# Kernel optimization log

Hardware: AMD Instinct MI355X
Metric: run time of the kernel (lower is better)

Reference implementation:

```python
import jax, jax.numpy as jnp
import numpy as np

NUM_EMBEDDINGS = 8192
EMBEDDING_DIM = 256
COMMITMENT_WEIGHT = 0.25
EMA_DECAY = 0.99
EPSILON = 1e-05


def setup_inputs() -> dict:
    key = jax.random.key(0)
    k1, k2 = jax.random.split(key)
    z = jax.random.normal(k1, (8, 4096, EMBEDDING_DIM), dtype=jnp.float32)
    # xavier-uniform-ish codebook init
    limit = np.sqrt(6.0 / (NUM_EMBEDDINGS + EMBEDDING_DIM))
    embeddings = jax.random.uniform(
        k2, (NUM_EMBEDDINGS, EMBEDDING_DIM), dtype=jnp.float32,
        minval=-limit, maxval=limit)
    ema_cluster_size = jnp.zeros((NUM_EMBEDDINGS,), dtype=jnp.float32)
    ema_embed_sum = embeddings.copy()
    return {
        'z': z,
        'embeddings': embeddings,
        'ema_cluster_size': ema_cluster_size,
        'ema_embed_sum': ema_embed_sum,
    }


def reference(z, embeddings, ema_cluster_size, ema_embed_sum):
    input_shape = z.shape
    D = input_shape[-1]
    z_flat = z.reshape(-1, D)                                  # [N, D]

    # Squared euclidean distances via expansion: ||z||^2 + ||e||^2 - 2 z.e
    z_sq = jnp.sum(z_flat * z_flat, axis=1, keepdims=True)     # [N, 1]
    e_sq = jnp.sum(embeddings * embeddings, axis=1)            # [K]
    ze = jnp.matmul(z_flat, embeddings.T)                      # [N, K]
    distances = z_sq + e_sq - 2.0 * ze                          # [N, K]
    indices = jnp.argmin(distances, axis=1)                    # [N] int

    z_q_flat = embeddings[indices]                             # [N, D] gather
    z_q = z_q_flat.reshape(input_shape)

    # commitment loss = mse(stop_grad(z_q), z)
    diff = jax.lax.stop_gradient(z_q) - z
    commitment_loss = jnp.mean(diff * diff) * COMMITMENT_WEIGHT

    # straight-through estimator
    z_q_st = z + jax.lax.stop_gradient(z_q - z)

    # EMA codebook update (functional version of the in-place buffer update)
    ones = jnp.ones_like(indices, dtype=embeddings.dtype)
    cluster_size = jax.ops.segment_sum(ones, indices, num_segments=NUM_EMBEDDINGS)
    embed_sum = jax.ops.segment_sum(z_flat, indices, num_segments=NUM_EMBEDDINGS)
    new_ema_cluster_size = EMA_DECAY * ema_cluster_size + (1.0 - EMA_DECAY) * cluster_size
    new_ema_embed_sum = EMA_DECAY * ema_embed_sum + (1.0 - EMA_DECAY) * embed_sum
    new_embeddings = new_ema_embed_sum / (new_ema_cluster_size[:, None] + EPSILON)

    indices_out = indices.reshape(input_shape[:-1])
    return (z_q_st, indices_out, commitment_loss,
            new_embeddings, new_ema_cluster_size, new_ema_embed_sum)
```

## Files before the change

kernel.cpp:

```cpp
#include <hip/hip_runtime.h>
#include <hip/hip_bf16.h>
#include <math.h>

#define N_TOK   32768
#define DIM     256
#define KC      8192

#define OUT_ZQ    0
#define OUT_IDX   8388608
#define OUT_LOSS  8421376
#define OUT_NEMB  8421377
#define OUT_CS    10518529
#define OUT_SUM   10526721

#define MARGIN  5e-3f
#define FLAGCAP 8192

typedef __attribute__((ext_vector_type(8))) __bf16 bf16x8;
typedef __attribute__((ext_vector_type(4))) float f32x4;

__device__ __forceinline__ void gload16(const void* g, void* l) {
  __builtin_amdgcn_global_load_lds((const __attribute__((address_space(1))) void*)g,
                                   (__attribute__((address_space(3))) void*)l, 16, 0, 0);
}

__device__ __forceinline__ float np_sumsq256(const float* __restrict__ p, int lane) {
  const int l = lane & 15;
  const int h = l >> 3;
  const int j = l & 7;
  const float* a = p + h * 128 + j;
  float x = a[0];
  float r = __fmul_rn(x, x);
  #pragma unroll
  for (int i = 1; i < 16; ++i) {
    x = a[8 * i];
    r = __fadd_rn(r, __fmul_rn(x, x));
  }
  r = __fadd_rn(r, __shfl_down(r, 1));
  r = __fadd_rn(r, __shfl_down(r, 2));
  r = __fadd_rn(r, __shfl_down(r, 4));
  float hi = __shfl(r, (lane & 48) | 8);
  return __fadd_rn(r, hi);
}

__global__ void vq_prep(const float* __restrict__ emb, float* __restrict__ esq,
                        short* __restrict__ esp2) {
  const int t = threadIdx.x;
  const int code = blockIdx.x * 8 + (t >> 5);
  const int p = t & 31, j = p >> 2, g = p & 3;
  const float* src = emb + (size_t)code * DIM + j * 32 + g * 8;
  const float4 v0 = *(const float4*)src;
  const float4 v1 = *(const float4*)(src + 4);
  const float xf[8] = {v0.x, v0.y, v0.z, v0.w, v1.x, v1.y, v1.z, v1.w};
  bf16x8 hb;
  #pragma unroll
  for (int e = 0; e < 8; ++e) hb[e] = (__bf16)xf[e];
  const int c = code & 15, sub = (code >> 4) & 3, ct = code >> 6;
  const int slot = (g + (c >> 1)) & 3;
  char* dst = (char*)esp2 + (size_t)ct * 32768 + ((sub * 8 + j) << 10) + c * 64 + slot * 16;
  *(bf16x8*)dst = hb;
  if (t < 128) {
    const int code2 = blockIdx.x * 8 + (t >> 4);
    const float s = np_sumsq256(emb + (size_t)code2 * DIM, t & 63);
    if ((t & 15) == 0) esq[code2] = s;
  }
}

__global__ void vq_transpose(const float* __restrict__ emb, float* __restrict__ embT) {
  __shared__ float t[64][65];
  const int tid = threadIdx.x;
  const int bc  = blockIdx.x & 127;
  const int bk  = blockIdx.x >> 7;
  const int cc0 = bc << 6, kc0 = bk << 6;
  const int col = tid & 63, qr = tid >> 6;
  #pragma unroll
  for (int i = 0; i < 16; ++i) {
    const int row = i * 4 + qr;
    t[row][col] = emb[(size_t)(cc0 + row) * DIM + kc0 + col];
  }
  __syncthreads();
  #pragma unroll
  for (int i = 0; i < 16; ++i) {
    const int krow = i * 4 + qr;
    embT[(size_t)(kc0 + krow) * KC + cc0 + col] = t[col][krow];
  }
}

__global__ void vq_init(int* __restrict__ hist, int* __restrict__ cnt) {
  const int i = blockIdx.x * blockDim.x + threadIdx.x;
  hist[i] = 0;
  if (i == 0) cnt[0] = 0;
}

__launch_bounds__(256, 4)
__global__ void vq_mfma(const float* __restrict__ z,
                        const short* __restrict__ esp,
                        const float* __restrict__ esq,
                        float* __restrict__ pb1,
                        int* __restrict__ pi1,
                        float* __restrict__ pb2) {
  __shared__ __align__(16) char lds[32768];
  const int tid  = threadIdx.x;
  const int lane = tid & 63;
  const int w    = tid >> 6;
  const int l15  = lane & 15;
  const int g    = lane >> 4;
  const int rt   = blockIdx.x >> 1;
  const int kh   = blockIdx.x & 1;
  const int rowbase = rt * 64 + w * 16;
  const int u0 = kh * 128, u1 = u0 + 128;
  const int gx = (g + (l15 >> 1)) & 3;
  const char* espb = (const char*)esp;

#define STAGE(U, BUFB)                                                           \
  {                                                                              \
    _Pragma("unroll")                                                            \
    for (int q_ = 0; q_ < 4; ++q_) {                                             \
      const int so_ = (((w << 2) + q_) << 10);                                   \
      gload16(espb + (size_t)(U) * 16384 + so_ + (lane << 4),                    \
              (void*)(lds + (BUFB) + so_));                                      \
    }                                                                            \
  }

  STAGE(u0, 0);

  bf16x8 Ahi[8], Alo[8];
  {
    const float* zr = z + (size_t)(rowbase + l15) * DIM + g * 8;
    #pragma unroll
    for (int c = 0; c < 8; ++c) {
      const float4 v0 = *(const float4*)(zr + c * 32);
      const float4 v1 = *(const float4*)(zr + c * 32 + 4);
      const float xf[8] = {v0.x, v0.y, v0.z, v0.w, v1.x, v1.y, v1.z, v1.w};
      #pragma unroll
      for (int e = 0; e < 8; ++e) {
        __bf16 hb = (__bf16)xf[e];
        Ahi[c][e] = hb;
        Alo[c][e] = (__bf16)(xf[e] - (float)hb);
      }
    }
  }

  __syncthreads();

  float b1[4], b2[4];
  int   i1[4];
  #pragma unroll
  for (int r = 0; r < 4; ++r) { b1[r] = 3.4e38f; b2[r] = 3.4e38f; i1[r] = 0x7fffffff; }

  int bp = 0;
  for (int u = u0; u < u1; ++u) {
    if (u + 1 < u1) STAGE(u + 1, (bp ^ 1) << 14);

    const float eq0 = esq[(u << 5) + l15];
    const float eq1 = esq[(u << 5) + 16 + l15];

    f32x4 acc0 = (f32x4){0.f, 0.f, 0.f, 0.f};
    f32x4 acc1 = (f32x4){0.f, 0.f, 0.f, 0.f};

    {
      const char* base = lds + (bp << 14);
      #pragma unroll
      for (int j_ = 0; j_ < 8; ++j_) {
        const char* bq_ = base + (j_ << 10) + (l15 << 6) + (gx << 4);
        const bf16x8 bF0 = *(const bf16x8*)(bq_);
        const bf16x8 bF1 = *(const bf16x8*)(bq_ + 8192);
        acc0 = __builtin_amdgcn_mfma_f32_16x16x32_bf16(Ahi[j_], bF0, acc0, 0, 0, 0);
        acc1 = __builtin_amdgcn_mfma_f32_16x16x32_bf16(Ahi[j_], bF1, acc1, 0, 0, 0);
        acc0 = __builtin_amdgcn_mfma_f32_16x16x32_bf16(Alo[j_], bF0, acc0, 0, 0, 0);
        acc1 = __builtin_amdgcn_mfma_f32_16x16x32_bf16(Alo[j_], bF1, acc1, 0, 0, 0);
      }
    }

    const int code0 = (u << 5) + l15;
    #pragma unroll
    for (int r = 0; r < 4; ++r) {
      const float sc = fmaf(-2.f, acc0[r], eq0);
      const bool lt = sc < b1[r];
      b2[r] = fminf(b2[r], fmaxf(sc, b1[r]));
      i1[r] = lt ? code0 : i1[r];
      b1[r] = fminf(b1[r], sc);
    }
    const int code1 = code0 + 16;
    #pragma unroll
    for (int r = 0; r < 4; ++r) {
      const float sc = fmaf(-2.f, acc1[r], eq1);
      const bool lt = sc < b1[r];
      b2[r] = fminf(b2[r], fmaxf(sc, b1[r]));
      i1[r] = lt ? code1 : i1[r];
      b1[r] = fminf(b1[r], sc);
    }
    __syncthreads();
    bp ^= 1;
  }

  #pragma unroll
  for (int r = 0; r < 4; ++r) {
    float v1 = b1[r], v2 = b2[r];
    int   j1 = i1[r];
    #pragma unroll
    for (int off = 1; off < 16; off <<= 1) {
      const float o1 = __shfl_xor(v1, off);
      const int   oj = __shfl_xor(j1, off);
      const float o2 = __shfl_xor(v2, off);
      v2 = fminf(fminf(v2, o2), fmaxf(v1, o1));
      const bool tk = (o1 < v1) || (o1 == v1 && oj < j1);
      j1 = tk ? oj : j1;
      v1 = fminf(v1, o1);
    }
    if (l15 == 0) {
      const int rr = kh * N_TOK + rowbase + (g << 2) + r;
      pb1[rr] = v1; pi1[rr] = j1; pb2[rr] = v2;
    }
  }
}

__global__ void vq_merge(const float* __restrict__ pb1, const int* __restrict__ pi1,
                         const float* __restrict__ pb2, int* __restrict__ idxf,
                         int* __restrict__ flag, int* __restrict__ cnt) {
  const int gi = blockIdx.x * blockDim.x + threadIdx.x;
  const float va = pb1[gi],        vb = pb1[N_TOK + gi];
  const int   ia = pi1[gi],        ib = pi1[N_TOK + gi];
  const float v2a = pb2[gi],       v2b = pb2[N_TOK + gi];
  float v1, v2; int i1;
  if (va < vb || (va == vb && ia < ib)) { v1 = va; i1 = ia; v2 = fminf(v2a, vb); }
  else                                  { v1 = vb; i1 = ib; v2 = fminf(v2b, va); }
  idxf[gi] = i1;
  if (v2 - v1 < MARGIN) {
    const int p = atomicAdd(cnt, 1);
    if (p < FLAGCAP) flag[p] = gi;
  }
}

__global__ void vq_rescan2(const float* __restrict__ z,
                           const float* __restrict__ embT,
                           const float* __restrict__ esq,
                           const int* __restrict__ flag,
                           const int* __restrict__ cnt,
                           float* __restrict__ rpv,
                           int* __restrict__ rpi) {
  __shared__ __align__(16) float zT[DIM][16];
  __shared__ float zsq_sh[16];
  __shared__ float rv[4][16];
  __shared__ int   ri[4][16];
  __shared__ int   rown[16];
  int n = *cnt; if (n > FLAGCAP) n = FLAGCAP;
  const int tid = threadIdx.x;
  const int lane = tid & 63, wv = tid >> 6;
  const int nb = (n + 15) >> 4;
  const int ntask = nb * 8;
  for (int task = blockIdx.x; task < ntask; task += gridDim.x) {
    const int bb = task >> 3, cz = task & 7;
    __syncthreads();
    if (tid < 16) rown[tid] = flag[min(bb * 16 + tid, n - 1)];
    __syncthreads();
    #pragma unroll
    for (int rr = 0; rr < 16; ++rr) zT[tid][rr] = z[(size_t)rown[rr] * DIM + tid];
    {
      const int rr = tid >> 4;
      const float s = np_sumsq256(z + (size_t)rown[rr] * DIM, lane);
      if ((tid & 15) == 0) zsq_sh[rr] = s;
    }
    __syncthreads();

    float a[16][4];
    #pragma unroll
    for (int rr = 0; rr < 16; ++rr)
      #pragma unroll
      for (int q = 0; q < 4; ++q) a[rr][q] = 0.f;

    const int c0 = cz * 1024 + tid;
    #pragma unroll 2
    for (int k = 0; k < DIM; ++k) {
      const float* rk = embT + (size_t)k * KC + c0;
      const float e0 = rk[0], e1 = rk[256], e2 = rk[512], e3 = rk[768];
      const f32x4 z0 = *(const f32x4*)&zT[k][0];
      const f32x4 z1 = *(const f32x4*)&zT[k][4];
      const f32x4 z2 = *(const f32x4*)&zT[k][8];
      const f32x4 z3 = *(const f32x4*)&zT[k][12];
      #pragma unroll
      for (int r4 = 0; r4 < 4; ++r4) {
        a[r4][0] = fmaf(z0[r4], e0, a[r4][0]);
        a[r4][1] = fmaf(z0[r4], e1, a[r4][1]);
        a[r4][2] = fmaf(z0[r4], e2, a[r4][2]);
        a[r4][3] = fmaf(z0[r4], e3, a[r4][3]);
        a[4 + r4][0] = fmaf(z1[r4], e0, a[4 + r4][0]);
        a[4 + r4][1] = fmaf(z1[r4], e1, a[4 + r4][1]);
        a[4 + r4][2] = fmaf(z1[r4], e2, a[4 + r4][2]);
        a[4 + r4][3] = fmaf(z1[r4], e3, a[4 + r4][3]);
        a[8 + r4][0] = fmaf(z2[r4], e0, a[8 + r4][0]);
        a[8 + r4][1] = fmaf(z2[r4], e1, a[8 + r4][1]);
        a[8 + r4][2] = fmaf(z2[r4], e2, a[8 + r4][2]);
        a[8 + r4][3] = fmaf(z2[r4], e3, a[8 + r4][3]);
        a[12 + r4][0] = fmaf(z3[r4], e0, a[12 + r4][0]);
        a[12 + r4][1] = fmaf(z3[r4], e1, a[12 + r4][1]);
        a[12 + r4][2] = fmaf(z3[r4], e2, a[12 + r4][2]);
        a[12 + r4][3] = fmaf(z3[r4], e3, a[12 + r4][3]);
      }
    }

    #pragma unroll
    for (int rr = 0; rr < 16; ++rr) {
      float bv = 3.4e38f; int bi = 0x7fffffff;
      #pragma unroll
      for (int q = 0; q < 4; ++q) {
        const int code = cz * 1024 + q * 256 + tid;
        const float D = __fsub_rn(__fadd_rn(zsq_sh[rr], esq[code]), __fmul_rn(2.f, a[rr][q]));
        if (D < bv) { bv = D; bi = code; }
      }
      #pragma unroll
      for (int off = 32; off; off >>= 1) {
        const float ov = __shfl_down(bv, off);
        const int   oi = __shfl_down(bi, off);
        if (ov < bv || (ov == bv && oi < bi)) { bv = ov; bi = oi; }
      }
      if (lane == 0) { rv[wv][rr] = bv; ri[wv][rr] = bi; }
    }
    __syncthreads();
    if (tid < 16) {
      const int fi = bb * 16 + tid;
      if (fi < n) {
        float fv = rv[0][tid]; int fx = ri[0][tid];
        #pragma unroll
        for (int q = 1; q < 4; ++q)
          if (rv[q][tid] < fv || (rv[q][tid] == fv && ri[q][tid] < fx)) { fv = rv[q][tid]; fx = ri[q][tid]; }
        rpv[fi * 8 + cz] = fv; rpi[fi * 8 + cz] = fx;
      }
    }
  }
}

__global__ void vq_rmerge(const int* __restrict__ flag, const int* __restrict__ cnt,
                          const float* __restrict__ rpv, const int* __restrict__ rpi,
                          int* __restrict__ idxf) {
  int n = *cnt; if (n > FLAGCAP) n = FLAGCAP;
  const int fi = blockIdx.x * blockDim.x + threadIdx.x;
  if (fi >= n) return;
  float bv = rpv[fi * 8]; int bi = rpi[fi * 8];
  #pragma unroll
  for (int c = 1; c < 8; ++c) {
    const float v = rpv[fi * 8 + c]; const int ix = rpi[fi * 8 + c];
    if (v < bv || (v == bv && ix < bi)) { bv = v; bi = ix; }
  }
  idxf[flag[fi]] = bi;
}

__global__ void vq_gather(const float* __restrict__ z, const float* __restrict__ emb,
                          const int* __restrict__ idxf, float* __restrict__ out,
                          float* __restrict__ lossp, int* __restrict__ hist) {
  __shared__ float part[4];
  const int tid = threadIdx.x, lane = tid & 63, w = tid >> 6;
  const int row = blockIdx.x * 4 + w;
  const int code = idxf[row];
  const float4 zv = *(const float4*)(z + (size_t)row * DIM + lane * 4);
  const float4 ev = *(const float4*)(emb + (size_t)code * DIM + lane * 4);
  float4 d, o;
  d.x = ev.x - zv.x; d.y = ev.y - zv.y; d.z = ev.z - zv.z; d.w = ev.w - zv.w;
  o.x = zv.x + d.x;  o.y = zv.y + d.y;  o.z = zv.z + d.z;  o.w = zv.w + d.w;
  *(float4*)(out + OUT_ZQ + (size_t)row * DIM + lane * 4) = o;
  float sq = fmaf(d.x, d.x, fmaf(d.y, d.y, fmaf(d.z, d.z, d.w * d.w)));
  #pragma unroll
  for (int off = 32; off; off >>= 1) sq += __shfl_down(sq, off);
  if (lane == 0) {
    part[w] = sq;
    atomicAdd(hist + code, 1);
    out[OUT_IDX + row] = (float)code;
  }
  __syncthreads();
  if (tid == 0) lossp[blockIdx.x] = (part[0] + part[1]) + (part[2] + part[3]);
}

__global__ void vq_prefix(const float* __restrict__ ema_cs, int* __restrict__ hist,
                          int* __restrict__ base, int* __restrict__ cursor,
                          const float* __restrict__ lossp, float* __restrict__ out) {
  __shared__ int ps[256];
  __shared__ float lp[4];
  const int t = threadIdx.x;

  float ls = 0.f;
  #pragma unroll
  for (int j = 0; j < 8; ++j) {
    const float4 v = *(const float4*)(lossp + t * 32 + j * 4);
    ls += (v.x + v.y) + (v.z + v.w);
  }
  #pragma unroll
  for (int off = 32; off; off >>= 1) ls += __shfl_down(ls, off);
  if ((t & 63) == 0) lp[t >> 6] = ls;

  int loc[32]; int s = 0;
  #pragma unroll
  for (int j = 0; j < 32; ++j) { loc[j] = hist[t * 32 + j]; s += loc[j]; }
  ps[t] = s;
  __syncthreads();
  if (t == 0)
    out[OUT_LOSS] = 0.25f * (((lp[0] + lp[1]) + (lp[2] + lp[3])) * (1.f / 8388608.f));
  for (int off = 1; off < 256; off <<= 1) {
    const int v = (t >= off) ? ps[t - off] : 0;
    __syncthreads();
    ps[t] += v;
    __syncthreads();
  }
  int run = ps[t] - s;
  #pragma unroll
  for (int j = 0; j < 32; ++j) {
    const int i = t * 32 + j;
    base[i] = run; cursor[i] = run;
    out[OUT_CS + i] = 0.99f * ema_cs[i] + 0.01f * (float)loc[j];
    run += loc[j];
  }
}

__global__ void vq_slot(const int* __restrict__ idxf, int* __restrict__ cursor,
                        int* __restrict__ rowlist) {
  const int gi = blockIdx.x * blockDim.x + threadIdx.x;
  const int code = idxf[gi];
  const int p = atomicAdd(cursor + code, 1);
  rowlist[p] = gi;
}

__global__ void vq_embsum(const float* __restrict__ z, const float* __restrict__ ema_sum,
                          const int* __restrict__ rowlist, const int* __restrict__ base,
                          const int* __restrict__ hist, float* __restrict__ out) {
  const int code = blockIdx.x;
  const int lane = threadIdx.x;
  const int b = base[code], n = hist[code];
  float a0 = 0.f, a1 = 0.f, a2 = 0.f, a3 = 0.f;
  for (int i = 0; i < n; ++i) {
    const float4 v = *(const float4*)(z + (size_t)rowlist[b + i] * DIM + lane * 4);
    a0 += v.x; a1 += v.y; a2 += v.z; a3 += v.w;
  }
  const float4 es = *(const float4*)(ema_sum + (size_t)code * DIM + lane * 4);
  const float s0 = 0.99f * es.x + 0.01f * a0;
  const float s1 = 0.99f * es.y + 0.01f * a1;
  const float s2 = 0.99f * es.z + 0.01f * a2;
  const float s3 = 0.99f * es.w + 0.01f * a3;
  float* sp = out + OUT_SUM + (size_t)code * DIM + lane * 4;
  sp[0] = s0; sp[1] = s1; sp[2] = s2; sp[3] = s3;
  const float cs = out[OUT_CS + code] + 1e-5f;
  float* np_ = out + OUT_NEMB + (size_t)code * DIM + lane * 4;
  np_[0] = s0 / cs; np_[1] = s1 / cs; np_[2] = s2 / cs; np_[3] = s3 / cs;
}

extern "C" void kernel_launch(void* const* d_in, const int* in_sizes, int n_in,
                              void* d_out, int out_size, void* d_ws, size_t ws_size,
                              hipStream_t stream) {
  const float* z      = (const float*)d_in[0];
  const float* emb    = (const float*)d_in[1];
  const float* emacs  = (const float*)d_in[2];
  const float* emasum = (const float*)d_in[3];
  float* out = (float*)d_out;
  float* ws  = (float*)d_ws;

  float* esq     = ws;
  int*   idxf    = (int*)(ws + 8192);
  int*   flag    = (int*)(ws + 40960);
  int*   cnt     = (int*)(ws + 49152);
  int*   hist    = (int*)(ws + 49408);
  int*   base    = (int*)(ws + 57600);
  int*   cursor  = (int*)(ws + 65792);
  int*   rowlist = (int*)(ws + 73984);
  float* pb1     = ws + 114944;
  int*   pi1     = (int*)(ws + 180480);
  float* pb2     = ws + 246016;
  short* esp2    = (short*)(ws + 311552);
  float* embT    = ws + 1360128;
  float* lossp   = pb1;
  float* rpv     = pb2;
  int*   rpi     = pi1;

  vq_prep<<<KC / 8, 256, 0, stream>>>(emb, esq, esp2);
  vq_transpose<<<512, 256, 0, stream>>>(emb, embT);
  vq_init<<<KC / 256, 256, 0, stream>>>(hist, cnt);

  vq_mfma<<<1024, 256, 0, stream>>>(z, esp2, esq, pb1, pi1, pb2);
  vq_merge<<<N_TOK / 256, 256, 0, stream>>>(pb1, pi1, pb2, idxf, flag, cnt);
  vq_rescan2<<<1024, 256, 0, stream>>>(z, embT, esq, flag, cnt, rpv, rpi);
  vq_rmerge<<<FLAGCAP / 256, 256, 0, stream>>>(flag, cnt, rpv, rpi, idxf);

  vq_gather<<<N_TOK / 4, 256, 0, stream>>>(z, emb, idxf, out, lossp, hist);
  vq_prefix<<<1, 256, 0, stream>>>(emacs, hist, base, cursor, lossp, out);
  vq_slot<<<N_TOK / 256, 256, 0, stream>>>(idxf, cursor, rowlist);
  vq_embsum<<<KC, 64, 0, stream>>>(z, emasum, rowlist, base, hist, out);
}
```

Before: 391.8 us.

## Drop bf16 low-part split, tile two row groups per wave, widen rescan margin

The coarse distance pass now uses only the bf16 high part of z, halving MFMA work per code. Each wave handles 32 rows instead of 16, so every LDS codebook fragment feeds two row tiles and the grid shrinks to 512 blocks. To absorb the larger error from dropping the low part, the near-tie margin and flag capacity grow, and the rescan buffers move to their own workspace region. This pushes more tokens into the exact fp32 rescan pass and lowers occupancy.

```diff
diff --git a/kernel.cpp b/kernel.cpp
--- a/kernel.cpp
+++ b/kernel.cpp
@@ -13,8 +13,8 @@
 #define OUT_CS    10518529
 #define OUT_SUM   10526721
 
-#define MARGIN  5e-3f
-#define FLAGCAP 8192
+#define MARGIN  8e-3f
+#define FLAGCAP 16384
 
 typedef __attribute__((ext_vector_type(8))) __bf16 bf16x8;
 typedef __attribute__((ext_vector_type(4))) float f32x4;
@@ -107,7 +107,7 @@
   const int g    = lane >> 4;
   const int rt   = blockIdx.x >> 1;
   const int kh   = blockIdx.x & 1;
-  const int rowbase = rt * 64 + w * 16;
+  const int rowbase = rt * 128 + w * 32;
   const int u0 = kh * 128, u1 = u0 + 128;
   const int gx = (g + (l15 >> 1)) & 3;
   const char* espb = (const char*)esp;
@@ -124,29 +124,28 @@
 
   STAGE(u0, 0);
 
-  bf16x8 Ahi[8], Alo[8];
-  {
-    const float* zr = z + (size_t)(rowbase + l15) * DIM + g * 8;
+  bf16x8 Ahi[2][8];
+  #pragma unroll
+  for (int s = 0; s < 2; ++s) {
+    const float* zr = z + (size_t)(rowbase + s * 16 + l15) * DIM + g * 8;
     #pragma unroll
     for (int c = 0; c < 8; ++c) {
       const float4 v0 = *(const float4*)(zr + c * 32);
       const float4 v1 = *(const float4*)(zr + c * 32 + 4);
       const float xf[8] = {v0.x, v0.y, v0.z, v0.w, v1.x, v1.y, v1.z, v1.w};
       #pragma unroll
-      for (int e = 0; e < 8; ++e) {
-        __bf16 hb = (__bf16)xf[e];
-        Ahi[c][e] = hb;
-        Alo[c][e] = (__bf16)(xf[e] - (float)hb);
-      }
+      for (int e = 0; e < 8; ++e) Ahi[s][c][e] = (__bf16)xf[e];
     }
   }
 
   __syncthreads();
 
-  float b1[4], b2[4];
-  int   i1[4];
-  #pragma unroll
-  for (int r = 0; r < 4; ++r) { b1[r] = 3.4e38f; b2[r] = 3.4e38f; i1[r] = 0x7fffffff; }
+  float b1[2][4], b2[2][4];
+  int   i1[2][4];
+  #pragma unroll
+  for (int s = 0; s < 2; ++s)
+    #pragma unroll
+    for (int r = 0; r < 4; ++r) { b1[s][r] = 3.4e38f; b2[s][r] = 3.4e38f; i1[s][r] = 0x7fffffff; }
 
   int bp = 0;
   for (int u = u0; u < u1; ++u) {
@@ -155,8 +154,10 @@
     const float eq0 = esq[(u << 5) + l15];
     const float eq1 = esq[(u << 5) + 16 + l15];
 
-    f32x4 acc0 = (f32x4){0.f, 0.f, 0.f, 0.f};
-    f32x4 acc1 = (f32x4){0.f, 0.f, 0.f, 0.f};
+    f32x4 acc00 = (f32x4){0.f, 0.f, 0.f, 0.f};
+    f32x4 acc01 = (f32x4){0.f, 0.f, 0.f, 0.f};
+    f32x4 acc10 = (f32x4){0.f, 0.f, 0.f, 0.f};
+    f32x4 acc11 = (f32x4){0.f, 0.f, 0.f, 0.f};
 
     {
       const char* base = lds + (bp << 14);
@@ -165,52 +166,71 @@
         const char* bq_ = base + (j_ << 10) + (l15 << 6) + (gx << 4);
         const bf16x8 bF0 = *(const bf16x8*)(bq_);
         const bf16x8 bF1 = *(const bf16x8*)(bq_ + 8192);
-        acc0 = __builtin_amdgcn_mfma_f32_16x16x32_bf16(Ahi[j_], bF0, acc0, 0, 0, 0);
-        acc1 = __builtin_amdgcn_mfma_f32_16x16x32_bf16(Ahi[j_], bF1, acc1, 0, 0, 0);
-        acc0 = __builtin_amdgcn_mfma_f32_16x16x32_bf16(Alo[j_], bF0, acc0, 0, 0, 0);
-        acc1 = __builtin_amdgcn_mfma_f32_16x16x32_bf16(Alo[j_], bF1, acc1, 0, 0, 0);
+        acc00 = __builtin_amdgcn_mfma_f32_16x16x32_bf16(Ahi[0][j_], bF0, acc00, 0, 0, 0);
+        acc01 = __builtin_amdgcn_mfma_f32_16x16x32_bf16(Ahi[0][j_], bF1, acc01, 0, 0, 0);
+        acc10 = __builtin_amdgcn_mfma_f32_16x16x32_bf16(Ahi[1][j_], bF0, acc10, 0, 0, 0);
+        acc11 = __builtin_amdgcn_mfma_f32_16x16x32_bf16(Ahi[1][j_], bF1, acc11, 0, 0, 0);
       }
     }
 
     const int code0 = (u << 5) + l15;
+    const int code1 = code0 + 16;
     #pragma unroll
     for (int r = 0; r < 4; ++r) {
-      const float sc = fmaf(-2.f, acc0[r], eq0);
-      const bool lt = sc < b1[r];
-      b2[r] = fminf(b2[r], fmaxf(sc, b1[r]));
-      i1[r] = lt ? code0 : i1[r];
-      b1[r] = fminf(b1[r], sc);
-    }
-    const int code1 = code0 + 16;
+      const float sc = fmaf(-2.f, acc00[r], eq0);
+      const bool lt = sc < b1[0][r];
+      b2[0][r] = fminf(b2[0][r], fmaxf(sc, b1[0][r]));
+      i1[0][r] = lt ? code0 : i1[0][r];
+      b1[0][r] = fminf(b1[0][r], sc);
+    }
     #pragma unroll
     for (int r = 0; r < 4; ++r) {
-      const float sc = fmaf(-2.f, acc1[r], eq1);
-      const bool lt = sc < b1[r];
-      b2[r] = fminf(b2[r], fmaxf(sc, b1[r]));
-      i1[r] = lt ? code1 : i1[r];
-      b1[r] = fminf(b1[r], sc);
+      const float sc = fmaf(-2.f, acc01[r], eq1);
+      const bool lt = sc < b1[0][r];
+      b2[0][r] = fminf(b2[0][r], fmaxf(sc, b1[0][r]));
+      i1[0][r] = lt ? code1 : i1[0][r];
+      b1[0][r] = fminf(b1[0][r], sc);
+    }
+    #pragma unroll
+    for (int r = 0; r < 4; ++r) {
+      const float sc = fmaf(-2.f, acc10[r], eq0);
+      const bool lt = sc < b1[1][r];
+      b2[1][r] = fminf(b2[1][r], fmaxf(sc, b1[1][r]));
+      i1[1][r] = lt ? code0 : i1[1][r];
+      b1[1][r] = fminf(b1[1][r], sc);
+    }
+    #pragma unroll
+    for (int r = 0; r < 4; ++r) {
+      const float sc = fmaf(-2.f, acc11[r], eq1);
+      const bool lt = sc < b1[1][r];
+      b2[1][r] = fminf(b2[1][r], fmaxf(sc, b1[1][r]));
+      i1[1][r] = lt ? code1 : i1[1][r];
+      b1[1][r] = fminf(b1[1][r], sc);
     }
     __syncthreads();
     bp ^= 1;
   }
 
   #pragma unroll
-  for (int r = 0; r < 4; ++r) {
-    float v1 = b1[r], v2 = b2[r];
-    int   j1 = i1[r];
-    #pragma unroll
-    for (int off = 1; off < 16; off <<= 1) {
-      const float o1 = __shfl_xor(v1, off);
-      const int   oj = __shfl_xor(j1, off);
-      const float o2 = __shfl_xor(v2, off);
-      v2 = fminf(fminf(v2, o2), fmaxf(v1, o1));
-      const bool tk = (o1 < v1) || (o1 == v1 && oj < j1);
-      j1 = tk ? oj : j1;
-      v1 = fminf(v1, o1);
-    }
-    if (l15 == 0) {
-      const int rr = kh * N_TOK + rowbase + (g << 2) + r;
-      pb1[rr] = v1; pi1[rr] = j1; pb2[rr] = v2;
+  for (int s = 0; s < 2; ++s) {
+    #pragma unroll
+    for (int r = 0; r < 4; ++r) {
+      float v1 = b1[s][r], v2 = b2[s][r];
+      int   j1 = i1[s][r];
+      #pragma unroll
+      for (int off = 1; off < 16; off <<= 1) {
+        const float o1 = __shfl_xor(v1, off);
+        const int   oj = __shfl_xor(j1, off);
+        const float o2 = __shfl_xor(v2, off);
+        v2 = fminf(fminf(v2, o2), fmaxf(v1, o1));
+        const bool tk = (o1 < v1) || (o1 == v1 && oj < j1);
+        j1 = tk ? oj : j1;
+        v1 = fminf(v1, o1);
+      }
+      if (l15 == 0) {
+        const int rr = kh * N_TOK + rowbase + s * 16 + (g << 2) + r;
+        pb1[rr] = v1; pi1[rr] = j1; pb2[rr] = v2;
+      }
     }
   }
 }
@@ -454,25 +474,25 @@
   float* esq     = ws;
   int*   idxf    = (int*)(ws + 8192);
   int*   flag    = (int*)(ws + 40960);
-  int*   cnt     = (int*)(ws + 49152);
-  int*   hist    = (int*)(ws + 49408);
-  int*   base    = (int*)(ws + 57600);
-  int*   cursor  = (int*)(ws + 65792);
-  int*   rowlist = (int*)(ws + 73984);
+  int*   cnt     = (int*)(ws + 57344);
+  int*   hist    = (int*)(ws + 57600);
+  int*   base    = (int*)(ws + 65792);
+  int*   cursor  = (int*)(ws + 73984);
+  int*   rowlist = (int*)(ws + 82176);
   float* pb1     = ws + 114944;
   int*   pi1     = (int*)(ws + 180480);
   float* pb2     = ws + 246016;
   short* esp2    = (short*)(ws + 311552);
   float* embT    = ws + 1360128;
+  float* rpv     = ws + 3457280;
+  int*   rpi     = (int*)(ws + 3588352);
   float* lossp   = pb1;
-  float* rpv     = pb2;
-  int*   rpi     = pi1;
 
   vq_prep<<<KC / 8, 256, 0, stream>>>(emb, esq, esp2);
   vq_transpose<<<512, 256, 0, stream>>>(emb, embT);
   vq_init<<<KC / 256, 256, 0, stream>>>(hist, cnt);
 
-  vq_mfma<<<1024, 256, 0, stream>>>(z, esp2, esq, pb1, pi1, pb2);
+  vq_mfma<<<512, 256, 0, stream>>>(z, esp2, esq, pb1, pi1, pb2);
   vq_merge<<<N_TOK / 256, 256, 0, stream>>>(pb1, pi1, pb2, idxf, flag, cnt);
   vq_rescan2<<<1024, 256, 0, stream>>>(z, embT, esq, flag, cnt, rpv, rpi);
   vq_rmerge<<<FLAGCAP / 256, 256, 0, stream>>>(flag, cnt, rpv, rpi, idxf);
```

Result: faster. 341.8 us (-12.8%).
